# Performance work log

Hardware: AMD Instinct MI355X
Metric: run time of the kernel (lower is better)

Reference implementation:

```python
import jax, jax.numpy as jnp
import numpy as np

S, N, C = 256, 512, 32   # n_seq, n_res, channels
EPS = 1e-3               # module eps for mask normalization
LN_EPS = 1e-5            # torch LayerNorm default eps


def setup_inputs() -> dict:
    key = jax.random.key(0)
    ks = jax.random.split(key, 6)
    scale = 1.0 / np.sqrt(C)
    return {
        "m": jax.random.normal(ks[0], (S, N, C), jnp.float32),
        "mask": jnp.ones((S, N), jnp.float32),
        "ln_gamma": jnp.ones((C,), jnp.float32),
        "ln_beta": jnp.zeros((C,), jnp.float32),
        "Wa": jax.random.normal(ks[1], (C, C), jnp.float32) * scale,
        "ba": jnp.zeros((C,), jnp.float32),
        "Wb": jax.random.normal(ks[2], (C, C), jnp.float32) * scale,
        "bb": jnp.zeros((C,), jnp.float32),
        "Wout": jax.random.normal(ks[3], (C * C, C), jnp.float32) * (1.0 / np.sqrt(C * C)),
        "bout": jnp.zeros((C,), jnp.float32),
    }


def reference(m, mask, ln_gamma, ln_beta, Wa, ba, Wb, bb, Wout, bout):
    # LayerNorm over channel dim
    mu = jnp.mean(m, axis=-1, keepdims=True)
    var = jnp.mean(jnp.square(m - mu), axis=-1, keepdims=True)
    mh = (m - mu) * jax.lax.rsqrt(var + LN_EPS) * ln_gamma + ln_beta  # [S, N, C]

    # dual linear projections, masked per (seq, res), then seq<->res transpose
    a = jnp.swapaxes((mh @ Wa + ba) * mask[..., None], -2, -3)  # [N, S, C]
    b = jnp.swapaxes((mh @ Wb + bb) * mask[..., None], -2, -3)  # [N, S, C]

    # outer product summed over sequences: [N, N, C, C] -> [N, N, C*C]
    outer = jnp.einsum("bac,dae->bdce", a, b).reshape(N, N, C * C)
    outer = outer @ Wout + bout  # [N, N, C]

    # pairwise mask normalization: sum over seqs of mask[s,i]*mask[s,j]
    norm = jnp.einsum("ab,ad->bd", mask, mask)[..., None] + EPS  # [N, N, 1]
    return outer / norm
```

## Files before the change

kernel.cpp:

```cpp
#include <hip/hip_runtime.h>

#define S_SEQ 256
#define N_RES 512
#define CCH   32

typedef __attribute__((ext_vector_type(8))) short bf16x8;
typedef __attribute__((ext_vector_type(4))) float f32x4;
typedef __attribute__((ext_vector_type(2))) unsigned int u32x2;

__device__ __forceinline__ unsigned short f2bf(float x) {
    unsigned int u = __float_as_uint(x);
    return (unsigned short)((u + 0x7FFFu + ((u >> 16) & 1u)) >> 16);
}

#define GLOAD_LDS16(gp, lp) __builtin_amdgcn_global_load_lds( \
    (const __attribute__((address_space(1))) unsigned int*)(gp), \
    (__attribute__((address_space(3))) unsigned int*)(lp), 16, 0, 0)

#define BAR()    do { __builtin_amdgcn_s_barrier(); asm volatile("" ::: "memory"); } while (0)
#define WLGKM0() asm volatile("s_waitcnt lgkmcnt(0)" ::: "memory")
#define WVM(n)   asm volatile("s_waitcnt vmcnt(" #n ")" ::: "memory")

__global__ __launch_bounds__(256) void prep_ab(
    const float* __restrict__ m, const float* __restrict__ mask,
    const float* __restrict__ gam, const float* __restrict__ bet,
    const float* __restrict__ Wa, const float* __restrict__ ba,
    const float* __restrict__ Wb, const float* __restrict__ bb,
    char* __restrict__ Ag, char* __restrict__ Bg)
{
    __shared__ float WaL[1024], WbL[1024];
    __shared__ float gL[32], btL[32], baL[32], bbL[32];
    __shared__ unsigned short At[32 * 256];
    __shared__ unsigned short Bt[32 * 256];

    const int n = blockIdx.x;
    const int t = threadIdx.x;

    for (int i = t; i < 1024; i += 256) { WaL[i] = Wa[i]; WbL[i] = Wb[i]; }
    if (t < 32) { gL[t] = gam[t]; btL[t] = bet[t]; baL[t] = ba[t]; bbL[t] = bb[t]; }
    __syncthreads();

    const int s = t;
    float mv[32];
    const float* mrow = m + ((size_t)s * N_RES + n) * CCH;
#pragma unroll
    for (int c4 = 0; c4 < 8; c4++) {
        f32x4 v = *(const f32x4*)(mrow + c4 * 4);
        mv[c4 * 4 + 0] = v.x; mv[c4 * 4 + 1] = v.y;
        mv[c4 * 4 + 2] = v.z; mv[c4 * 4 + 3] = v.w;
    }
    float mu = 0.f;
#pragma unroll
    for (int c = 0; c < 32; c++) mu += mv[c];
    mu *= (1.f / 32.f);
    float var = 0.f;
#pragma unroll
    for (int c = 0; c < 32; c++) { float d = mv[c] - mu; var += d * d; }
    var *= (1.f / 32.f);
    float rs = rsqrtf(var + 1e-5f);
    float mh[32];
#pragma unroll
    for (int c = 0; c < 32; c++) mh[c] = (mv[c] - mu) * rs * gL[c] + btL[c];

    const float msk = mask[(size_t)s * N_RES + n];

    f32x4 av[8], bv[8];
#pragma unroll
    for (int cg = 0; cg < 8; cg++) { av[cg] = (f32x4)0.f; bv[cg] = (f32x4)0.f; }
#pragma unroll
    for (int k = 0; k < 32; k++) {
        float x = mh[k];
#pragma unroll
        for (int cg = 0; cg < 8; cg++) {
            f32x4 wa4 = *(const f32x4*)&WaL[k * 32 + cg * 4];
            f32x4 wb4 = *(const f32x4*)&WbL[k * 32 + cg * 4];
            av[cg] += x * wa4;
            bv[cg] += x * wb4;
        }
    }
#pragma unroll
    for (int cg = 0; cg < 8; cg++) {
#pragma unroll
        for (int u = 0; u < 4; u++) {
            int c = cg * 4 + u;
            At[c * 256 + s] = f2bf((av[cg][u] + baL[c]) * msk);
            Bt[c * 256 + s] = f2bf((bv[cg][u] + bbL[c]) * msk);
        }
    }
    __syncthreads();

    const size_t taA = (size_t)(n >> 2) * 65536;
    const size_t taB = (size_t)(n >> 3) * 131072;
    const int irb = (n & 3) * 32;
    const int halfB = (n >> 2) & 1;
#pragma unroll
    for (int u = 0; u < 4; u++) {
        int cid = t * 4 + u;
        int c = cid >> 5, g = cid & 31;
        int kt = g >> 2, q = g & 3;
        size_t offA = taA + (size_t)kt * 8192
                    + (size_t)(irb + c) * 64 + (size_t)((q ^ (c & 3)) << 4);
        size_t offB = taB + (size_t)kt * 16384
                    + (size_t)(irb + c) * 128
                    + (size_t)((((halfB << 2) | q) ^ (c & 7)) << 4);
        *(uint4*)(Ag + offA) = *(const uint4*)(At + c * 256 + g * 8);
        *(uint4*)(Bg + offB) = *(const uint4*)(Bt + c * 256 + g * 8);
    }
}

__global__ __launch_bounds__(256) void kwt(const float* __restrict__ Wout,
                                           unsigned short* __restrict__ Wt3)
{
    int idx = blockIdx.x * 256 + threadIdx.x;
    int e = idx >> 10, ch = (idx >> 5) & 31, c = idx & 31;
    Wt3[idx] = f2bf(Wout[(size_t)(c * 32 + e) * 32 + ch]);
}

__global__ __launch_bounds__(256) void knorm(const float* __restrict__ mask,
                                             float* __restrict__ inv_norm)
{
    __shared__ float Mi[64][65];
    __shared__ float Mj[64][65];
    const int bi = blockIdx.x >> 3, bj = blockIdx.x & 7;
    const int t = threadIdx.x;
    const int ty = t >> 4, tx = t & 15;

    float acc[4][4];
#pragma unroll
    for (int a = 0; a < 4; a++)
#pragma unroll
        for (int b = 0; b < 4; b++) acc[a][b] = 0.f;

    for (int sc = 0; sc < 4; sc++) {
        for (int e = t; e < 4096; e += 256) {
            int sr = e >> 6, col = e & 63;
            Mi[sr][col] = mask[(size_t)(sc * 64 + sr) * N_RES + bi * 64 + col];
            Mj[sr][col] = mask[(size_t)(sc * 64 + sr) * N_RES + bj * 64 + col];
        }
        __syncthreads();
        for (int sp = 0; sp < 64; sp++) {
#pragma unroll
            for (int a = 0; a < 4; a++)
#pragma unroll
                for (int b = 0; b < 4; b++)
                    acc[a][b] += Mi[sp][ty * 4 + a] * Mj[sp][tx * 4 + b];
        }
        __syncthreads();
    }
#pragma unroll
    for (int a = 0; a < 4; a++)
#pragma unroll
        for (int b = 0; b < 4; b++) {
            int i = bi * 64 + ty * 4 + a;
            int j = bj * 64 + tx * 4 + b;
            inv_norm[(size_t)i * N_RES + j] = 1.f / (acc[a][b] + 1e-3f);
        }
}

__global__ __launch_bounds__(512, 4) void kmain7(
    const char* __restrict__ Ag, const char* __restrict__ Bg,
    const unsigned short* __restrict__ Wt3, const float* __restrict__ inv_norm,
    const float* __restrict__ bout, float* __restrict__ out)
{
    __shared__ __align__(16) char sm[66048];

    const int bid = blockIdx.x;
    const int xcd = bid & 7;
    const int xidx = bid >> 3;
    const int chunk = xidx >> 8;
    const int TI = xcd * 16 + ((xidx >> 4) & 15);
    const int TJ = chunk * 16 + (xidx & 15);

    const int t = threadIdx.x;
    const int lane = t & 63, wid = t >> 6;
    const int wr = wid >> 2, wc = wid & 3;
    const int rl = lane & 15, h4 = lane >> 4;

    const char* pa = Ag + (size_t)TI * 65536;
    const char* pb = Bg + (size_t)TJ * 131072;

#define SH(kt) do { \
    char* db_ = sm + (((kt) & 1) * 24576); \
    GLOAD_LDS16(pa + (kt) * 8192 + t * 16,         db_ + t * 16); \
    GLOAD_LDS16(pb + (kt) * 16384 + t * 16,        db_ + 8192 + t * 16); \
    GLOAD_LDS16(pb + (kt) * 16384 + 8192 + t * 16, db_ + 16384 + t * 16); \
} while (0)

    const int abase = (wr * 64 + rl) * 64 + ((h4 ^ (rl & 3)) << 4);
    const int bbase = 8192 + ((wc & 1) * 64 + rl) * 128
                    + (((((wc >> 1) << 2) | h4) ^ (rl & 7)) << 4);

    f32x4 acc[4][4];
#pragma unroll
    for (int a = 0; a < 4; a++)
#pragma unroll
        for (int b = 0; b < 4; b++) acc[a][b] = (f32x4)0.f;

    SH(0);
    SH(1);

#pragma unroll
    for (int kt = 0; kt < 8; kt++) {
        if (kt < 7) { WVM(3); } else { WVM(0); }
        BAR();
        const char* buf = sm + ((kt & 1) * 24576);
        bf16x8 af[4], bfr[4];
#pragma unroll
        for (int am = 0; am < 4; am++)
            af[am] = *(const bf16x8*)(buf + abase + am * 1024);
#pragma unroll
        for (int bn = 0; bn < 4; bn++)
            bfr[bn] = *(const bf16x8*)(buf + bbase + bn * 2048);
        WLGKM0();
        __builtin_amdgcn_s_setprio(1);
#pragma unroll
        for (int am = 0; am < 4; am++)
#pragma unroll
            for (int bn = 0; bn < 4; bn++)
                acc[am][bn] = __builtin_amdgcn_mfma_f32_16x16x32_bf16(
                    af[am], bfr[bn], acc[am][bn], 0, 0, 0);
        __builtin_amdgcn_s_setprio(0);
        BAR();
        if (kt <= 5) SH(kt + 2);
    }
#undef SH

#pragma unroll
    for (int am = 0; am < 4; am++) {
        const int lpr = (am >> 1) * 8 + wc * 2;
        const int cs = ((am & 1) << 1) + (h4 >> 1);
#pragma unroll
        for (int bn = 0; bn < 4; bn++) {
            const int lp = lpr + (bn >> 1);
            const int e = ((bn & 1) << 4) + rl;
            unsigned int lo = (unsigned int)f2bf(acc[am][bn][0]) |
                              ((unsigned int)f2bf(acc[am][bn][1]) << 16);
            unsigned int hi = (unsigned int)f2bf(acc[am][bn][2]) |
                              ((unsigned int)f2bf(acc[am][bn][3]) << 16);
            u32x2 wv; wv[0] = lo; wv[1] = hi;
            *(u32x2*)(sm + wr * 33024 + lp * 2064 + e * 64 +
                      ((cs ^ (e & 3)) << 4) + ((h4 & 1) << 3)) = wv;
        }
    }
    WLGKM0();
    BAR();

    const int slotR = wid >> 2, kq = wid & 3;
    f32x4 ae0 = (f32x4)0.f, ae1 = (f32x4)0.f;
    const char* grow = sm + slotR * 33024 + rl * 2064;
#pragma unroll
    for (int es = 0; es < 8; es++) {
        const int e = kq * 8 + es;
        bf16x8 ga = *(const bf16x8*)(grow + e * 64 + ((h4 ^ (e & 3)) << 4));
        bf16x8 wb0 = *(const bf16x8*)(Wt3 + (size_t)e * 1024 + rl * 32 + h4 * 8);
        bf16x8 wb1 = *(const bf16x8*)(Wt3 + (size_t)e * 1024 + (16 + rl) * 32 + h4 * 8);
        ae0 = __builtin_amdgcn_mfma_f32_16x16x32_bf16(ga, wb0, ae0, 0, 0, 0);
        ae1 = __builtin_amdgcn_mfma_f32_16x16x32_bf16(ga, wb1, ae1, 0, 0, 0);
    }
    WLGKM0();
    BAR();

    float* ps = (float*)sm;
#pragma unroll
    for (int r = 0; r < 4; r++) {
        ps[((slotR * 4 + kq) * 16 + h4 * 4 + r) * 34 + rl]      = ae0[r];
        ps[((slotR * 4 + kq) * 16 + h4 * 4 + r) * 34 + 16 + rl] = ae1[r];
    }
    WLGKM0();
    BAR();

#pragma unroll
    for (int u = 0; u < 2; u++) {
        const int idx = u * 512 + t;
        const int p = idx >> 5, ch = idx & 31;
        float v = 0.f;
#pragma unroll
        for (int k2 = 0; k2 < 4; k2++)
            v += ps[(((p >> 4) * 4 + k2) * 16 + (p & 15)) * 34 + ch];
        const int i = TI * 4 + (p >> 3), j = TJ * 8 + (p & 7);
        out[((size_t)(i * N_RES + j)) * CCH + ch] =
            (v + bout[ch]) * inv_norm[(size_t)i * N_RES + j];
    }
}

extern "C" void kernel_launch(void* const* d_in, const int* in_sizes, int n_in,
                              void* d_out, int out_size, void* d_ws, size_t ws_size,
                              hipStream_t stream)
{
    const float* m    = (const float*)d_in[0];
    const float* mask = (const float*)d_in[1];
    const float* gam  = (const float*)d_in[2];
    const float* bet  = (const float*)d_in[3];
    const float* Wa   = (const float*)d_in[4];
    const float* ba   = (const float*)d_in[5];
    const float* Wb   = (const float*)d_in[6];
    const float* bb   = (const float*)d_in[7];
    const float* Wout = (const float*)d_in[8];
    const float* bout = (const float*)d_in[9];
    float* out = (float*)d_out;

    char* ws = (char*)d_ws;
    char* Ag = ws;
    char* Bg = ws + 8388608;
    unsigned short* Wt3 = (unsigned short*)(ws + 16777216);
    float* inv_norm = (float*)(ws + 16842752);

    prep_ab<<<dim3(N_RES), dim3(256), 0, stream>>>(m, mask, gam, bet, Wa, ba, Wb, bb, Ag, Bg);
    kwt<<<dim3(128), dim3(256), 0, stream>>>(Wout, Wt3);
    knorm<<<dim3(64), dim3(256), 0, stream>>>(mask, inv_norm);
    kmain7<<<dim3(8192), dim3(512), 0, stream>>>(Ag, Bg, Wt3, inv_norm, bout, out);
}
```

Baseline: 210.4 us.

## Shrink main outer-product tile to 4x4 residue pairs with 256-thread blocks

Changes the main kernel tile from 4x8 residue pairs per 512-thread block to 4x4 pairs per 256-thread block. The A and B staging layouts become identical 128-byte-row swizzled tiles, and prep_ab writes both with one offset. LDS use drops to about 33 KB, so more blocks can be resident per CU and twice as many blocks are launched. In exchange, each B tile is loaded more often from global memory because there is less reuse per block.

```diff
diff --git a/kernel.cpp b/kernel.cpp
--- a/kernel.cpp
+++ b/kernel.cpp
@@ -89,22 +89,18 @@
     }
     __syncthreads();
 
-    const size_t taA = (size_t)(n >> 2) * 65536;
-    const size_t taB = (size_t)(n >> 3) * 131072;
-    const int irb = (n & 3) * 32;
-    const int halfB = (n >> 2) & 1;
+    const size_t tbase = (size_t)(n >> 2) * 65536;
+    const int halfq = ((n >> 1) & 1) << 2;
+    const int irb = (n & 1) * 32;
 #pragma unroll
     for (int u = 0; u < 4; u++) {
         int cid = t * 4 + u;
         int c = cid >> 5, g = cid & 31;
         int kt = g >> 2, q = g & 3;
-        size_t offA = taA + (size_t)kt * 8192
-                    + (size_t)(irb + c) * 64 + (size_t)((q ^ (c & 3)) << 4);
-        size_t offB = taB + (size_t)kt * 16384
-                    + (size_t)(irb + c) * 128
-                    + (size_t)((((halfB << 2) | q) ^ (c & 7)) << 4);
-        *(uint4*)(Ag + offA) = *(const uint4*)(At + c * 256 + g * 8);
-        *(uint4*)(Bg + offB) = *(const uint4*)(Bt + c * 256 + g * 8);
+        size_t off = tbase + (size_t)kt * 8192 + (size_t)(irb + c) * 128
+                   + (size_t)(((halfq | q) ^ (c & 7)) << 4);
+        *(uint4*)(Ag + off) = *(const uint4*)(At + c * 256 + g * 8);
+        *(uint4*)(Bg + off) = *(const uint4*)(Bt + c * 256 + g * 8);
     }
 }
 
@@ -157,38 +153,37 @@
         }
 }
 
-__global__ __launch_bounds__(512, 4) void kmain7(
+__global__ __launch_bounds__(256, 4) void kmain8(
     const char* __restrict__ Ag, const char* __restrict__ Bg,
     const unsigned short* __restrict__ Wt3, const float* __restrict__ inv_norm,
     const float* __restrict__ bout, float* __restrict__ out)
 {
-    __shared__ __align__(16) char sm[66048];
+    __shared__ __align__(16) char sm[33024];
 
     const int bid = blockIdx.x;
     const int xcd = bid & 7;
     const int xidx = bid >> 3;
-    const int chunk = xidx >> 8;
-    const int TI = xcd * 16 + ((xidx >> 4) & 15);
-    const int TJ = chunk * 16 + (xidx & 15);
+    const int TI = xcd * 16 + ((xidx >> 5) & 15);
+    const int TJ = (xidx >> 9) * 32 + (xidx & 31);
 
     const int t = threadIdx.x;
     const int lane = t & 63, wid = t >> 6;
-    const int wr = wid >> 2, wc = wid & 3;
+    const int wr = wid >> 1, wc = wid & 1;
     const int rl = lane & 15, h4 = lane >> 4;
 
     const char* pa = Ag + (size_t)TI * 65536;
-    const char* pb = Bg + (size_t)TJ * 131072;
+    const char* pb = Bg + (size_t)TJ * 65536;
 
 #define SH(kt) do { \
-    char* db_ = sm + (((kt) & 1) * 24576); \
-    GLOAD_LDS16(pa + (kt) * 8192 + t * 16,         db_ + t * 16); \
-    GLOAD_LDS16(pb + (kt) * 16384 + t * 16,        db_ + 8192 + t * 16); \
-    GLOAD_LDS16(pb + (kt) * 16384 + 8192 + t * 16, db_ + 16384 + t * 16); \
+    char* db_ = sm + (((kt) & 1) * 16384); \
+    GLOAD_LDS16(pa + (kt) * 8192 + t * 16,        db_ + t * 16); \
+    GLOAD_LDS16(pa + (kt) * 8192 + 4096 + t * 16, db_ + 4096 + t * 16); \
+    GLOAD_LDS16(pb + (kt) * 8192 + t * 16,        db_ + 8192 + t * 16); \
+    GLOAD_LDS16(pb + (kt) * 8192 + 4096 + t * 16, db_ + 12288 + t * 16); \
 } while (0)
 
-    const int abase = (wr * 64 + rl) * 64 + ((h4 ^ (rl & 3)) << 4);
-    const int bbase = 8192 + ((wc & 1) * 64 + rl) * 128
-                    + (((((wc >> 1) << 2) | h4) ^ (rl & 7)) << 4);
+    const int abase = rl * 128 + (((((wr << 2) | h4)) ^ (rl & 7)) << 4);
+    const int bbase = 8192 + rl * 128 + (((((wc << 2) | h4)) ^ (rl & 7)) << 4);
 
     f32x4 acc[4][4];
 #pragma unroll
@@ -201,13 +196,13 @@
 
 #pragma unroll
     for (int kt = 0; kt < 8; kt++) {
-        if (kt < 7) { WVM(3); } else { WVM(0); }
+        if (kt < 7) { WVM(4); } else { WVM(0); }
         BAR();
-        const char* buf = sm + ((kt & 1) * 24576);
+        const char* buf = sm + ((kt & 1) * 16384);
         bf16x8 af[4], bfr[4];
 #pragma unroll
         for (int am = 0; am < 4; am++)
-            af[am] = *(const bf16x8*)(buf + abase + am * 1024);
+            af[am] = *(const bf16x8*)(buf + abase + am * 2048);
 #pragma unroll
         for (int bn = 0; bn < 4; bn++)
             bfr[bn] = *(const bf16x8*)(buf + bbase + bn * 2048);
@@ -227,27 +222,26 @@
 
 #pragma unroll
     for (int am = 0; am < 4; am++) {
-        const int lpr = (am >> 1) * 8 + wc * 2;
         const int cs = ((am & 1) << 1) + (h4 >> 1);
 #pragma unroll
         for (int bn = 0; bn < 4; bn++) {
-            const int lp = lpr + (bn >> 1);
+            const int p = (wr * 2 + (am >> 1)) * 4 + wc * 2 + (bn >> 1);
             const int e = ((bn & 1) << 4) + rl;
             unsigned int lo = (unsigned int)f2bf(acc[am][bn][0]) |
                               ((unsigned int)f2bf(acc[am][bn][1]) << 16);
             unsigned int hi = (unsigned int)f2bf(acc[am][bn][2]) |
                               ((unsigned int)f2bf(acc[am][bn][3]) << 16);
             u32x2 wv; wv[0] = lo; wv[1] = hi;
-            *(u32x2*)(sm + wr * 33024 + lp * 2064 + e * 64 +
+            *(u32x2*)(sm + p * 2064 + e * 64 +
                       ((cs ^ (e & 3)) << 4) + ((h4 & 1) << 3)) = wv;
         }
     }
     WLGKM0();
     BAR();
 
-    const int slotR = wid >> 2, kq = wid & 3;
+    const int kq = wid;
     f32x4 ae0 = (f32x4)0.f, ae1 = (f32x4)0.f;
-    const char* grow = sm + slotR * 33024 + rl * 2064;
+    const char* grow = sm + rl * 2064;
 #pragma unroll
     for (int es = 0; es < 8; es++) {
         const int e = kq * 8 + es;
@@ -263,21 +257,21 @@
     float* ps = (float*)sm;
 #pragma unroll
     for (int r = 0; r < 4; r++) {
-        ps[((slotR * 4 + kq) * 16 + h4 * 4 + r) * 34 + rl]      = ae0[r];
-        ps[((slotR * 4 + kq) * 16 + h4 * 4 + r) * 34 + 16 + rl] = ae1[r];
+        ps[(kq * 16 + h4 * 4 + r) * 34 + rl]      = ae0[r];
+        ps[(kq * 16 + h4 * 4 + r) * 34 + 16 + rl] = ae1[r];
     }
     WLGKM0();
     BAR();
 
 #pragma unroll
     for (int u = 0; u < 2; u++) {
-        const int idx = u * 512 + t;
+        const int idx = u * 256 + t;
         const int p = idx >> 5, ch = idx & 31;
         float v = 0.f;
 #pragma unroll
         for (int k2 = 0; k2 < 4; k2++)
-            v += ps[(((p >> 4) * 4 + k2) * 16 + (p & 15)) * 34 + ch];
-        const int i = TI * 4 + (p >> 3), j = TJ * 8 + (p & 7);
+            v += ps[(k2 * 16 + p) * 34 + ch];
+        const int i = TI * 4 + (p >> 2), j = TJ * 4 + (p & 3);
         out[((size_t)(i * N_RES + j)) * CCH + ch] =
             (v + bout[ch]) * inv_norm[(size_t)i * N_RES + j];
     }
@@ -308,5 +302,5 @@
     prep_ab<<<dim3(N_RES), dim3(256), 0, stream>>>(m, mask, gam, bet, Wa, ba, Wb, bb, Ag, Bg);
     kwt<<<dim3(128), dim3(256), 0, stream>>>(Wout, Wt3);
     knorm<<<dim3(64), dim3(256), 0, stream>>>(mask, inv_norm);
-    kmain7<<<dim3(8192), dim3(512), 0, stream>>>(Ag, Bg, Wt3, inv_norm, bout, out);
-}
+    kmain8<<<dim3(16384), dim3(256), 0, stream>>>(Ag, Bg, Wt3, inv_norm, bout, out);
+}
```

Measured after the change: 205.4 us. 2.4% less time.
